# Kernel tuning notes

Measured on AMD Instinct MI355X. Metric: run time of the kernel, lower is better.

The kernel has to match this reference:

```python
import jax, jax.numpy as jnp
import numpy as np

# Math note: feat = cat([ctx_i, asp_j, ctx_i*asp_j]) dotted with w_u [6H,1]
# decomposes as ctx_i.w1 + asp_j.w2 + (ctx_i*asp_j).w3 where w_u = cat([w1,w2,w3]).
# This lets us compute the full [B, L1, L2] alignment matrix with three small
# contractions instead of L1*L2 concat+matmul launches, with identical math.

def setup_inputs() -> dict:
    key = jax.random.key(0)
    k1, k2, k3 = jax.random.split(key, 3)
    B, L1, L2, D = 64, 512, 32, 600  # D = 2*hidden_dim
    ctx = jax.random.normal(k1, (B, L1, D), dtype=jnp.float32)
    asp = jax.random.normal(k2, (B, L2, D), dtype=jnp.float32)
    w_u = jax.random.normal(k3, (3 * D, 1), dtype=jnp.float32)
    return {"batch_size": B, "ctx": ctx, "asp": asp, "w_u": w_u}

def reference(batch_size, ctx, asp, w_u):
    D = ctx.shape[-1]
    w = w_u[:, 0]
    w1, w2, w3 = w[:D], w[D:2 * D], w[2 * D:]
    ctx_term = ctx @ w1                                  # [B, L1]
    asp_term = asp @ w2                                  # [B, L2]
    cross = jnp.einsum('bid,bjd->bij', ctx * w3, asp)    # [B, L1, L2]
    return ctx_term[:, :, None] + asp_term[:, None, :] + cross
```

## Files before the change

kernel.cpp:

```cpp
#include <hip/hip_runtime.h>
#include <hip/hip_bf16.h>

typedef float  f32x4  __attribute__((ext_vector_type(4)));
typedef short  bf16x8 __attribute__((ext_vector_type(8)));
typedef short  s16x4  __attribute__((ext_vector_type(4)));

#define NB   64
#define NL1  512
#define NL2  32
#define ND   600
#define NDP  640
#define NW1  608
#define ROWS 64

static __device__ __forceinline__ short f2bf(float f) {
    __hip_bfloat16 h = __float2bfloat16(f);
    return __builtin_bit_cast(short, h);
}

__global__ __launch_bounds__(256, 2)
void align_kernel(const float* __restrict__ ctx,
                  const float* __restrict__ asp,
                  const float* __restrict__ wu,
                  float* __restrict__ out)
{
    __shared__ short aspw3[NL2 * NDP];
    __shared__ short w1bf[NW1];
    __shared__ float aspterm[NL2];

    const int tid     = threadIdx.x;
    const int lane    = tid & 63;
    const int wid     = tid >> 6;
    const int b       = blockIdx.x;
    const int rowbase = blockIdx.y * ROWS;

    const int r16 = lane & 15;
    const int g   = lane >> 4;
    const int jx  = lane & 7;
    const float* actx = ctx + ((size_t)b * NL1 + rowbase + wid * 16 + r16) * ND + 8 * g;

    float4 a0 = *(const float4*)(actx);       float4 b0 = *(const float4*)(actx + 4);
    float4 a1 = *(const float4*)(actx + 32);  float4 b1 = *(const float4*)(actx + 36);
    float4 a2 = *(const float4*)(actx + 64);  float4 b2 = *(const float4*)(actx + 68);
    float4 a3 = *(const float4*)(actx + 96);  float4 b3 = *(const float4*)(actx + 100);

    for (int i = tid; i < NW1; i += 256)
        w1bf[i] = (i < ND) ? f2bf(wu[i]) : (short)0;

    {
        const int j   = tid >> 3;
        const int e   = tid & 7;
        const int jxs = j & 7;

        aspw3[j * NDP + ((75 ^ jxs) << 3) + e] = 0;

        const int sub = tid & 7;
        const float* arow = asp + ((size_t)b * NL2 + j) * ND;
        float at = 0.f;
        #pragma unroll
        for (int m = 0; m < 19; ++m) {
            const int k = m * 32 + sub * 4;
            if (k < ND) {
                const float4 v  = *(const float4*)(arow + k);
                const float4 w2 = *(const float4*)(wu + ND + k);
                const float4 w3 = *(const float4*)(wu + 2 * ND + k);
                at += v.x * w2.x + v.y * w2.y + v.z * w2.z + v.w * w2.w;
                s16x4 h;
                h.x = f2bf(v.x * w3.x);
                h.y = f2bf(v.y * w3.y);
                h.z = f2bf(v.z * w3.z);
                h.w = f2bf(v.w * w3.w);
                const int c = (k >> 3) ^ jxs;
                *(s16x4*)&aspw3[j * NDP + (c << 3) + (k & 7)] = h;
            }
        }
        at += __shfl_xor(at, 1);
        at += __shfl_xor(at, 2);
        at += __shfl_xor(at, 4);
        if (sub == 0) aspterm[j] = at;
    }
    __syncthreads();

    f32x4 acc0 = {0.f, 0.f, 0.f, 0.f};
    f32x4 acc1 = {0.f, 0.f, 0.f, 0.f};
    f32x4 acc2 = {0.f, 0.f, 0.f, 0.f};

#define PIPE_STEP(u, aU, bU)                                                   \
    {                                                                          \
        const int s = s0 + (u);                                                \
        if (s < 19) {                                                          \
            const int t = s + 4;                                               \
            float4 p0, p1;                                                     \
            if ((t <= 17) || (t == 18 && g < 3)) {                             \
                p0 = *(const float4*)(actx + t * 32);                          \
                p1 = *(const float4*)(actx + t * 32 + 4);                      \
            } else {                                                           \
                p0 = make_float4(0.f, 0.f, 0.f, 0.f);                          \
                p1 = make_float4(0.f, 0.f, 0.f, 0.f);                          \
            }                                                                  \
            bf16x8 af;                                                         \
            af[0] = f2bf(aU.x); af[1] = f2bf(aU.y);                            \
            af[2] = f2bf(aU.z); af[3] = f2bf(aU.w);                            \
            af[4] = f2bf(bU.x); af[5] = f2bf(bU.y);                            \
            af[6] = f2bf(bU.z); af[7] = f2bf(bU.w);                            \
            const int c = ((s * 4 + g) ^ jx) << 3;                             \
            const bf16x8 f0 = *(const bf16x8*)&aspw3[r16 * NDP + c];           \
            const bf16x8 f1 = *(const bf16x8*)&aspw3[(16 + r16) * NDP + c];    \
            const bf16x8 wf = *(const bf16x8*)&w1bf[s * 32 + 8 * g];           \
            acc0 = __builtin_amdgcn_mfma_f32_16x16x32_bf16(af, f0, acc0, 0, 0, 0); \
            acc1 = __builtin_amdgcn_mfma_f32_16x16x32_bf16(af, f1, acc1, 0, 0, 0); \
            acc2 = __builtin_amdgcn_mfma_f32_16x16x32_bf16(af, wf, acc2, 0, 0, 0); \
            aU = p0; bU = p1;                                                  \
        }                                                                      \
    }

    #pragma unroll 1
    for (int s0 = 0; s0 < 19; s0 += 4) {
        PIPE_STEP(0, a0, b0)
        PIPE_STEP(1, a1, b1)
        PIPE_STEP(2, a2, b2)
        PIPE_STEP(3, a3, b3)
    }
#undef PIPE_STEP

    const float atj0 = aspterm[r16];
    const float atj1 = aspterm[16 + r16];
    float* orow = out + ((size_t)b * NL1 + rowbase + wid * 16 + g * 4) * NL2;
    #pragma unroll
    for (int r = 0; r < 4; ++r) {
        const float cterm = acc2[r];
        orow[r * NL2 + r16]      = acc0[r] + cterm + atj0;
        orow[r * NL2 + 16 + r16] = acc1[r] + cterm + atj1;
    }
}

extern "C" void kernel_launch(void* const* d_in, const int* in_sizes, int n_in,
                              void* d_out, int out_size, void* d_ws, size_t ws_size,
                              hipStream_t stream) {
    (void)in_sizes; (void)n_in; (void)d_ws; (void)ws_size; (void)out_size;
    const float* ctx = (const float*)d_in[1];
    const float* asp = (const float*)d_in[2];
    const float* wu  = (const float*)d_in[3];
    float* out = (float*)d_out;
    dim3 grid(NB, NL1 / ROWS);
    align_kernel<<<grid, 256, 0, stream>>>(ctx, asp, wu, out);
}
```

Before: 21.65 us.

## Stage ctx slabs through swizzled LDS with coalesced row-wise global loads

Changes how each wave reads its 16 ctx rows. Eight lanes now read one row's 128 contiguous bytes per load, instead of each lane fetching two strided float4 pieces per row. The slabs are written into a per-wave, XOR-swizzled, double-buffered LDS tile and read back in MFMA fragment layout, with a three-slab register prefetch rotation. The aim is better global-load coalescing on this bandwidth-heavy kernel. The cost is extra LDS writes and reads per step and a shorter prefetch distance than the previous four-step register pipeline.

After: 21.65 us. About the same (-0.0%).

```diff
diff --git a/kernel.cpp b/kernel.cpp
--- a/kernel.cpp
+++ b/kernel.cpp
@@ -27,6 +27,7 @@
     __shared__ short aspw3[NL2 * NDP];
     __shared__ short w1bf[NW1];
     __shared__ float aspterm[NL2];
+    __shared__ float ctxs[4][2][16][32];
 
     const int tid     = threadIdx.x;
     const int lane    = tid & 63;
@@ -37,12 +38,35 @@
     const int r16 = lane & 15;
     const int g   = lane >> 4;
     const int jx  = lane & 7;
-    const float* actx = ctx + ((size_t)b * NL1 + rowbase + wid * 16 + r16) * ND + 8 * g;
+    const int r7  = r16 & 7;
 
-    float4 a0 = *(const float4*)(actx);       float4 b0 = *(const float4*)(actx + 4);
-    float4 a1 = *(const float4*)(actx + 32);  float4 b1 = *(const float4*)(actx + 36);
-    float4 a2 = *(const float4*)(actx + 64);  float4 b2 = *(const float4*)(actx + 68);
-    float4 a3 = *(const float4*)(actx + 96);  float4 b3 = *(const float4*)(actx + 100);
+    const int lr = lane >> 3;
+    const int lc = lane & 7;
+    const float* ctx_base = ctx + ((size_t)b * NL1 + rowbase + wid * 16) * ND;
+
+#define LOADSLAB(t, A0, A1) do {                                               \
+        if ((t) <= 18) {                                                       \
+            if ((t) == 18 && lc >= 6) {                                        \
+                A0 = (f32x4){0.f,0.f,0.f,0.f};                                 \
+                A1 = (f32x4){0.f,0.f,0.f,0.f};                                 \
+            } else {                                                           \
+                A0 = *(const f32x4*)(ctx_base + (size_t)lr * ND     + (t)*32 + lc*4); \
+                A1 = *(const f32x4*)(ctx_base + (size_t)(8+lr) * ND + (t)*32 + lc*4); \
+            }                                                                  \
+        }                                                                      \
+    } while (0)
+
+#define WRITESLAB(t, A0, A1) do {                                              \
+        if ((t) <= 18) {                                                       \
+            *(f32x4*)&ctxs[wid][(t)&1][lr]  [(lc ^ lr) * 4] = A0;              \
+            *(f32x4*)&ctxs[wid][(t)&1][8+lr][(lc ^ lr) * 4] = A1;              \
+        }                                                                      \
+    } while (0)
+
+    f32x4 P0a, P0b, P1a, P1b, P2a, P2b;
+    LOADSLAB(0, P0a, P0b);
+    LOADSLAB(1, P1a, P1b);
+    LOADSLAB(2, P2a, P2b);
 
     for (int i = tid; i < NW1; i += 256)
         w1bf[i] = (i < ND) ? f2bf(wu[i]) : (short)0;
@@ -79,49 +103,45 @@
         at += __shfl_xor(at, 4);
         if (sub == 0) aspterm[j] = at;
     }
+
+    WRITESLAB(0, P0a, P0b);
     __syncthreads();
 
-    f32x4 acc0 = {0.f, 0.f, 0.f, 0.f};
-    f32x4 acc1 = {0.f, 0.f, 0.f, 0.f};
-    f32x4 acc2 = {0.f, 0.f, 0.f, 0.f};
+    f32x4 acc0 = {0,0,0,0};
+    f32x4 acc1 = {0,0,0,0};
+    f32x4 acc2 = {0,0,0,0};
 
-#define PIPE_STEP(u, aU, bU)                                                   \
-    {                                                                          \
-        const int s = s0 + (u);                                                \
-        if (s < 19) {                                                          \
-            const int t = s + 4;                                               \
-            float4 p0, p1;                                                     \
-            if ((t <= 17) || (t == 18 && g < 3)) {                             \
-                p0 = *(const float4*)(actx + t * 32);                          \
-                p1 = *(const float4*)(actx + t * 32 + 4);                      \
-            } else {                                                           \
-                p0 = make_float4(0.f, 0.f, 0.f, 0.f);                          \
-                p1 = make_float4(0.f, 0.f, 0.f, 0.f);                          \
-            }                                                                  \
-            bf16x8 af;                                                         \
-            af[0] = f2bf(aU.x); af[1] = f2bf(aU.y);                            \
-            af[2] = f2bf(aU.z); af[3] = f2bf(aU.w);                            \
-            af[4] = f2bf(bU.x); af[5] = f2bf(bU.y);                            \
-            af[6] = f2bf(bU.z); af[7] = f2bf(bU.w);                            \
-            const int c = ((s * 4 + g) ^ jx) << 3;                             \
-            const bf16x8 f0 = *(const bf16x8*)&aspw3[r16 * NDP + c];           \
-            const bf16x8 f1 = *(const bf16x8*)&aspw3[(16 + r16) * NDP + c];    \
-            const bf16x8 wf = *(const bf16x8*)&w1bf[s * 32 + 8 * g];           \
-            acc0 = __builtin_amdgcn_mfma_f32_16x16x32_bf16(af, f0, acc0, 0, 0, 0); \
-            acc1 = __builtin_amdgcn_mfma_f32_16x16x32_bf16(af, f1, acc1, 0, 0, 0); \
-            acc2 = __builtin_amdgcn_mfma_f32_16x16x32_bf16(af, wf, acc2, 0, 0, 0); \
-            aU = p0; bU = p1;                                                  \
-        }                                                                      \
-    }
+#define STEP(s, LA0, LA1, WA0, WA1) do {                                       \
+        LOADSLAB((s)+3, LA0, LA1);                                             \
+        const f32x4 fa = *(const f32x4*)&ctxs[wid][(s)&1][r16][((2*g    ) ^ r7) * 4]; \
+        const f32x4 fb = *(const f32x4*)&ctxs[wid][(s)&1][r16][((2*g + 1) ^ r7) * 4]; \
+        bf16x8 af;                                                             \
+        af[0] = f2bf(fa.x); af[1] = f2bf(fa.y); af[2] = f2bf(fa.z); af[3] = f2bf(fa.w); \
+        af[4] = f2bf(fb.x); af[5] = f2bf(fb.y); af[6] = f2bf(fb.z); af[7] = f2bf(fb.w); \
+        const int cB = (((s) * 4 + g) ^ jx) << 3;                              \
+        const bf16x8 f0 = *(const bf16x8*)&aspw3[r16 * NDP + cB];              \
+        const bf16x8 f1 = *(const bf16x8*)&aspw3[(16 + r16) * NDP + cB];       \
+        const bf16x8 wf = *(const bf16x8*)&w1bf[(s) * 32 + 8 * g];             \
+        acc0 = __builtin_amdgcn_mfma_f32_16x16x32_bf16(af, f0, acc0, 0, 0, 0); \
+        acc1 = __builtin_amdgcn_mfma_f32_16x16x32_bf16(af, f1, acc1, 0, 0, 0); \
+        acc2 = __builtin_amdgcn_mfma_f32_16x16x32_bf16(af, wf, acc2, 0, 0, 0); \
+        WRITESLAB((s)+1, WA0, WA1);                                            \
+    } while (0)
 
     #pragma unroll 1
-    for (int s0 = 0; s0 < 19; s0 += 4) {
-        PIPE_STEP(0, a0, b0)
-        PIPE_STEP(1, a1, b1)
-        PIPE_STEP(2, a2, b2)
-        PIPE_STEP(3, a3, b3)
+    for (int m = 0; m < 18; m += 6) {
+        STEP(m + 0, P0a, P0b, P1a, P1b);
+        STEP(m + 1, P1a, P1b, P2a, P2b);
+        STEP(m + 2, P2a, P2b, P0a, P0b);
+        STEP(m + 3, P0a, P0b, P1a, P1b);
+        STEP(m + 4, P1a, P1b, P2a, P2b);
+        STEP(m + 5, P2a, P2b, P0a, P0b);
     }
-#undef PIPE_STEP
+    STEP(18, P0a, P0b, P1a, P1b);
+
+#undef STEP
+#undef WRITESLAB
+#undef LOADSLAB
 
     const float atj0 = aspterm[r16];
     const float atj1 = aspterm[16 + r16];
```
